# Kernel optimization log

Measured on AMD Instinct MI355X. Metric: run time of the kernel, lower is better.

## Reference

```python
import jax, jax.numpy as jnp
import numpy as np

NQ = 16  # nqubits
BATCH = 256

def _ry(t):
    # t: (...,) real angles -> (..., 2, 2) complex64 Ry(t)
    c = jnp.cos(t / 2).astype(jnp.complex64)
    s = jnp.sin(t / 2).astype(jnp.complex64)
    return jnp.stack([jnp.stack([c, -s], -1), jnp.stack([s, c], -1)], -2)

def _rz(t):
    # diag(e^{-i t/2}, e^{i t/2})
    e0 = jnp.exp(-0.5j * t.astype(jnp.complex64))
    e1 = jnp.exp(0.5j * t.astype(jnp.complex64))
    z = jnp.zeros_like(e0)
    return jnp.stack([jnp.stack([e0, z], -1), jnp.stack([z, e1], -1)], -2)

def _apply_1q(st, g, w):
    # st: (B, 2^n) complex, g: (2,2) or (B,2,2); wire w (0 = most significant, matching kron order)
    B = st.shape[0]
    x = st.reshape(B, 2 ** w, 2, -1)
    if g.ndim == 3:
        x = jnp.einsum('iab,ilbr->ilar', g, x)
    else:
        x = jnp.einsum('ab,ilbr->ilar', g, x)
    return x.reshape(B, -1)

def _apply_cnot(st, c, t, n):
    # CNOT(control=c, target=t): flip target bit where control bit == 1
    B = st.shape[0]
    x = st.reshape((B,) + (2,) * n)
    c_ax = c + 1
    ctrl0 = jnp.take(x, 0, axis=c_ax)
    ctrl1 = jnp.take(x, 1, axis=c_ax)
    t_ax = t + 1 if t < c else t  # target axis index after removing control axis
    ctrl1 = jnp.flip(ctrl1, axis=t_ax)  # flip along size-2 axis == Pauli-X
    x = jnp.stack([ctrl0, ctrl1], axis=c_ax)
    return x.reshape(B, -1)

def _yzy(st, w3, n):
    # per-qubit Ry(a) Rz(b) Ry(c); params laid out (n, 3) applied in order a, b, c
    p = w3.reshape(n, 3)
    g = jnp.einsum('nab,nbc,ncd->nad', _ry(p[:, 2]), _rz(p[:, 1]), _ry(p[:, 0]))
    for i in range(n):
        st = _apply_1q(st, g[i], i)
    return st

def _ring(st, step, n):
    # ring_of_cnot (step=1) / ring_of_cnot2 (step=2)
    for i in range(n):
        st = _apply_cnot(st, i, (i + step) % n, n)
    return st

def _forward(inputs, weight):
    B, n = inputs.shape
    # |0...0> initial state, batched
    st = jnp.zeros((B, 2 ** n), jnp.complex64).at[:, 0].set(1.0)
    # PauliEncoding with pauli='Y': Ry(inputs[:, i]) on wire i (batched gate)
    enc = _ry(inputs)  # (B, n, 2, 2)
    for i in range(n):
        st = _apply_1q(st, enc[:, i], i)
    # BasicEntangleLayer x2 = YZY + ring_of_cnot
    st = _yzy(st, weight[0 * n:3 * n], n); st = _ring(st, 1, n)
    st = _yzy(st, weight[3 * n:6 * n], n); st = _ring(st, 1, n)
    # YZY, ring_of_cnot2, YZY, ring_of_cnot2, YZY
    st = _yzy(st, weight[6 * n:9 * n], n); st = _ring(st, 2, n)
    st = _yzy(st, weight[9 * n:12 * n], n); st = _ring(st, 2, n)
    st = _yzy(st, weight[12 * n:15 * n], n)
    # <Z_i> = sum_probs(bit_i=0) - sum_probs(bit_i=1); output scaled by 4 as in original
    probs = st.real ** 2 + st.imag ** 2  # (B, 2^n) real
    z = []
    for i in range(n):
        p = probs.reshape(B, 2 ** i, 2, -1)
        z.append((p[:, :, 0, :] - p[:, :, 1, :]).sum(axis=(1, 2)))
    return jnp.stack(z, axis=1) * 4.0  # (B, n)

def setup_inputs() -> dict:
    key = jax.random.key(0)
    k1, k2 = jax.random.split(key)
    inputs = jax.random.uniform(k1, (BATCH, NQ), jnp.float32, 0.0, 2.0 * np.pi)
    weight = jax.random.uniform(k2, (15 * NQ,), jnp.float32, 0.0, 2.0 * np.pi)
    return {"inputs": inputs, "weight": weight}

def reference(inputs, weight):
    return _forward(inputs, weight)
```

## Files before the change

kernel.cpp:

```cpp
#include <hip/hip_runtime.h>
#include <hip/hip_fp16.h>
#include <utility>
#include <type_traits>


constexpr int NSR  = 88;
constexpr int NGRR = 22;
constexpr int NGL  = 10;
constexpr int NG   = 32;

struct M16 { unsigned r[16]; };

constexpr M16 ident() { M16 m{}; for (int i = 0; i < 16; ++i) m.r[i] = 1u << i; return m; }

constexpr M16 ringm(int s) {
  M16 m = ident();
  for (int i = 15; i >= 0; --i) {
    int pc = 15 - i;
    int pt = 15 - ((i + s) & 15);
    m.r[pt] ^= m.r[pc];
  }
  return m;
}

constexpr M16 mmul(M16 A, M16 B) {
  M16 C{};
  for (int p = 0; p < 16; ++p) {
    unsigned v = 0;
    for (int q = 0; q < 16; ++q) if ((A.r[p] >> q) & 1u) v ^= B.r[q];
    C.r[p] = v;
  }
  return C;
}

constexpr M16 minv(M16 A) {
  M16 I = ident();
  for (int col = 0; col < 16; ++col) {
    int piv = -1;
    for (int row = col; row < 16; ++row) if ((A.r[row] >> col) & 1u) { piv = row; break; }
    unsigned t = A.r[piv]; A.r[piv] = A.r[col]; A.r[col] = t;
    t = I.r[piv]; I.r[piv] = I.r[col]; I.r[col] = t;
    for (int row = 0; row < 16; ++row)
      if (row != col && ((A.r[row] >> col) & 1u)) { A.r[row] ^= A.r[col]; I.r[row] ^= I.r[col]; }
  }
  return I;
}

constexpr bool meq(M16 a, M16 b) { for (int i = 0; i < 16; ++i) if (a.r[i] != b.r[i]) return false; return true; }
constexpr unsigned colmask(M16 P, int b) { unsigned m = 0; for (int p = 0; p < 16; ++p) m |= ((P.r[p] >> b) & 1u) << p; return m; }
constexpr int popc16(unsigned x) { int c = 0; for (int i = 0; i < 16; ++i) c += (x >> i) & 1; return c; }
constexpr int topbit_pow(unsigned x) { int b = 0; for (int i = 0; i < 16; ++i) if ((x >> i) & 1) b = i; return 1 << b; }

struct Tables { unsigned gm[64]; unsigned gc[64]; unsigned meas[16]; };

constexpr Tables make_tables() {
  Tables T{};
  M16 R1 = ringm(1), R2 = ringm(2);
  M16 P0 = R1;
  M16 P1 = mmul(R1, R1);
  M16 P2 = mmul(P1, R2);
  M16 P3 = mmul(P2, R2);
  M16 P[4] = { P0, P1, P2, P3 };
  for (int k = 0; k < 4; ++k) {
    M16 A = minv(P[k]);
    for (int b = 0; b < 16; ++b) {
      T.gm[k * 16 + b] = colmask(P[k], b);
      T.gc[k * 16 + b] = A.r[b];
    }
  }
  M16 A5 = minv(P[3]);
  for (int w = 0; w < 16; ++w) T.meas[w] = A5.r[15 - w];
  return T;
}

constexpr Tables TB = make_tables();

constexpr bool check_tables() {
  for (int g = 0; g < 64; ++g) if ((popc16(TB.gm[g] & TB.gc[g]) & 1) != 1) return false;
  if (!meq(mmul(ringm(1), minv(ringm(1))), ident())) return false;
  if (!meq(mmul(ringm(2), minv(ringm(2))), ident())) return false;
  return true;
}
static_assert(check_tables(), "GF(2) table inconsistency");
static_assert(sizeof(__half2) == 4, "half2 size");

template<int N, int I = 0, typename F>
__device__ __forceinline__ void sfor(F&& f) {
  if constexpr (I < N) {
    f(std::integral_constant<int, I>{});
    sfor<N, I + 1>(static_cast<F&&>(f));
  }
}

__device__ __forceinline__ int h2i(__half2 v) { return __builtin_bit_cast(int, v); }
__device__ __forceinline__ __half2 i2h(int v) { return __builtin_bit_cast(__half2, v); }
__device__ __forceinline__ unsigned h2u(__half2 v) { return __builtin_bit_cast(unsigned, v); }
__device__ __forceinline__ __half2 u2h(unsigned v) { return __builtin_bit_cast(__half2, v); }

template<int T>
__device__ __forceinline__ __half2 upd(__half2 xs_, __half2 xp_,
                                       __half2 c0_, __half2 c1_, __half2 c2_, __half2 c3_) {
  const unsigned xs = h2u(xs_), xp = h2u(xp_);
  const unsigned c0 = h2u(c0_), c1 = h2u(c1_), c2 = h2u(c2_), c3 = h2u(c3_);
  unsigned y;
  if constexpr (T) {
    asm("v_pk_mul_f16 %0, %1, %2\n\t"
        "v_pk_fma_f16 %0, %3, %2, %0 op_sel:[0,1,0] op_sel_hi:[1,0,1] neg_lo:[1,0,0] neg_hi:[1,0,0]\n\t"
        "v_pk_fma_f16 %0, %4, %5, %0 neg_lo:[1,0,0] neg_hi:[1,0,0]\n\t"
        "v_pk_fma_f16 %0, %6, %5, %0 op_sel:[0,1,0] op_sel_hi:[1,0,1]"
        : "=&v"(y)
        : "v"(c0), "v"(xs), "v"(c1), "v"(c2), "v"(xp), "v"(c3));
  } else {
    asm("v_pk_mul_f16 %0, %1, %2\n\t"
        "v_pk_fma_f16 %0, %3, %2, %0 op_sel:[0,1,0] op_sel_hi:[1,0,1]\n\t"
        "v_pk_fma_f16 %0, %4, %5, %0\n\t"
        "v_pk_fma_f16 %0, %6, %5, %0 op_sel:[0,1,0] op_sel_hi:[1,0,1]"
        : "=&v"(y)
        : "v"(c0), "v"(xs), "v"(c1), "v"(c2), "v"(xp), "v"(c3));
  }
  return u2h(y);
}

template<int lx>
__device__ __forceinline__ __half2 pget(__half2 v) {
  if constexpr (lx == 0) return v;
  else return i2h(__shfl_xor(h2i(v), lx, 64));
}

__device__ __forceinline__ void su2_coeffs(float a, float b, float c,
                                           float& are, float& aim, float& bre, float& bim) {
  float sapc, capc, samc, camc, sb, cb;
  __sincosf((a + c) * 0.5f, &sapc, &capc);
  __sincosf((a - c) * 0.5f, &samc, &camc);
  __sincosf(b * 0.5f, &sb, &cb);
  are = cb * capc;
  aim = -sb * camc;
  bre = cb * sapc;
  bim = sb * samc;
}

__device__ __forceinline__ unsigned pkh2(float lo, float hi) {
  return h2u(__floats2half2_rn(lo, hi));
}

__device__ __forceinline__ float2 cmulf(float2 a, float vr, float vi) {
  return make_float2(a.x * vr - a.y * vi, a.x * vi + a.y * vr);
}

template<int G>
__device__ __forceinline__ void vg_load(const __half2 (&S)[NSR], const uint4* sg4,
                                        unsigned tid, __half2 (&a)[4]) {
  if constexpr (G < NGRR) {
    a[0] = S[4*G]; a[1] = S[4*G+1]; a[2] = S[4*G+2]; a[3] = S[4*G+3];
  } else {
    const uint4 v = sg4[(G - NGRR) * 512 + tid];
    a[0] = u2h(v.x); a[1] = u2h(v.y); a[2] = u2h(v.z); a[3] = u2h(v.w);
  }
}
template<int G>
__device__ __forceinline__ void vg_store(__half2 (&S)[NSR], uint4* sg4,
                                         unsigned tid, const __half2 (&a)[4]) {
  if constexpr (G < NGRR) {
    S[4*G] = a[0]; S[4*G+1] = a[1]; S[4*G+2] = a[2]; S[4*G+3] = a[3];
  } else {
    sg4[(G - NGRR) * 512 + tid] = make_uint4(h2u(a[0]), h2u(a[1]), h2u(a[2]), h2u(a[3]));
  }
}
template<int G>
__device__ __forceinline__ uint4 vg_pack(const __half2 (&S)[NSR], const uint4* sg4, unsigned tid) {
  if constexpr (G < NGRR)
    return make_uint4(h2u(S[4*G]), h2u(S[4*G+1]), h2u(S[4*G+2]), h2u(S[4*G+3]));
  else
    return sg4[(G - NGRR) * 512 + tid];
}

template<int G, int me, unsigned cm>
__device__ __forceinline__ void vg_upd(__half2 (&S)[NSR], uint4* sg4, unsigned tid, uint4 pv,
                                       __half2 c0, __half2 c1, __half2 c2, __half2 c3) {
  const unsigned q[4] = { pv.x, pv.y, pv.z, pv.w };
  __half2 a[4]; vg_load<G>(S, sg4, tid, a);
  sfor<4>([&](auto ee) {
    constexpr int e = decltype(ee)::value;
    constexpr int L = 4 * G + e;
    constexpr int t = popc16(cm & (unsigned)L) & 1;
    a[e] = upd<t>(a[e], u2h(q[e ^ me]), c0, c1, c2, c3);
  });
  vg_store<G>(S, sg4, tid, a);
}

template<int G>
__device__ __forceinline__ void apply_gate(__half2 (&S)[NSR], unsigned tid,
                                           const uint4* __restrict__ ctabg,
                                           uint4* sg4, uint4* xbuf4) {
  constexpr unsigned m  = TB.gm[G];
  constexpr unsigned c  = TB.gc[G];
  constexpr unsigned mL = m & 127u;
  constexpr unsigned mT = m >> 7;
  constexpr unsigned mW = m >> 13;

  const uint4 cc = ctabg[G];
  const unsigned fm = (__popc((c >> 7) & tid) & 1u) ? 0x80008000u : 0u;
  const __half2 c0 = u2h(cc.x), c1 = u2h(cc.y ^ fm), c2 = u2h(cc.z ^ fm), c3 = u2h(cc.w);

  if constexpr (mW == 0u) {
    constexpr int lx = (int)mT;
    if constexpr (mL == 0u) {
      sfor<NG>([&](auto gg) {
        constexpr int g = decltype(gg)::value;
        __half2 a[4]; vg_load<g>(S, sg4, tid, a);
        sfor<4>([&](auto ee) {
          constexpr int e = decltype(ee)::value;
          constexpr int L = 4*g + e;
          constexpr int t = popc16(c & (unsigned)L) & 1;
          a[e] = upd<t>(a[e], pget<lx>(a[e]), c0, c1, c2, c3);
        });
        vg_store<g>(S, sg4, tid, a);
      });
    } else if constexpr ((mL >> 2) == 0u) {
      constexpr int tb = topbit_pow(mL);
      sfor<NG>([&](auto gg) {
        constexpr int g = decltype(gg)::value;
        __half2 a[4]; vg_load<g>(S, sg4, tid, a);
        sfor<4>([&](auto ee) {
          constexpr int e = decltype(ee)::value;
          if constexpr ((e & tb) == 0) {
            constexpr int e1 = e ^ (int)mL;
            constexpr int L0 = 4*g + e, L1 = 4*g + e1;
            constexpr int t0 = popc16(c & (unsigned)L0) & 1;
            constexpr int t1 = popc16(c & (unsigned)L1) & 1;
            const __half2 x0 = a[e], x1 = a[e1];
            a[e]  = upd<t0>(x0, pget<lx>(x1), c0, c1, c2, c3);
            a[e1] = upd<t1>(x1, pget<lx>(x0), c0, c1, c2, c3);
          }
        });
        vg_store<g>(S, sg4, tid, a);
      });
    } else {
      constexpr int hg = (int)(mL >> 2);
      constexpr int tb = topbit_pow((unsigned)hg);
      constexpr int me = (int)(mL & 3u);
      sfor<NG>([&](auto ga_) {
        constexpr int gA = decltype(ga_)::value;
        if constexpr ((gA & tb) == 0) {
          constexpr int gB = gA ^ hg;
          __half2 a[4], b4[4];
          vg_load<gA>(S, sg4, tid, a); vg_load<gB>(S, sg4, tid, b4);
          sfor<4>([&](auto ee) {
            constexpr int e  = decltype(ee)::value;
            constexpr int e2 = e ^ me;
            constexpr int L0 = 4*gA + e, L1 = 4*gB + e2;
            constexpr int t0 = popc16(c & (unsigned)L0) & 1;
            constexpr int t1 = popc16(c & (unsigned)L1) & 1;
            const __half2 x0 = a[e], x1 = b4[e2];
            a[e]   = upd<t0>(x0, pget<lx>(x1), c0, c1, c2, c3);
            b4[e2] = upd<t1>(x1, pget<lx>(x0), c0, c1, c2, c3);
          });
          vg_store<gA>(S, sg4, tid, a); vg_store<gB>(S, sg4, tid, b4);
        }
      });
    }
  } else {
    const unsigned ptid = tid ^ (unsigned)mT;
    constexpr unsigned hG = mL >> 2;
    constexpr int      me = (int)(mL & 3u);
    if constexpr (hG == 0u) {
      sfor<4>([&](auto rr) {
        constexpr int r = decltype(rr)::value;
        sfor<8>([&](auto kk) {
          constexpr int k = decltype(kk)::value;
          xbuf4[tid * 9u + (unsigned)k] = vg_pack<r * 8 + k>(S, sg4, tid);
        });
        __syncthreads();
        sfor<8>([&](auto kk) {
          constexpr int k = decltype(kk)::value;
          const uint4 pv = xbuf4[ptid * 9u + (unsigned)k];
          vg_upd<r * 8 + k, me, c>(S, sg4, tid, pv, c0, c1, c2, c3);
        });
        __syncthreads();
      });
    } else {
      constexpr int tbG = topbit_pow(hG);
      sfor<4>([&](auto rr) {
        constexpr int r = decltype(rr)::value;
        sfor<4>([&](auto kk) {
          constexpr int k  = decltype(kk)::value;
          constexpr int i  = r * 4 + k;
          constexpr int gA = ((i & ~(tbG - 1)) << 1) | (i & (tbG - 1));
          constexpr int gB = gA ^ (int)hG;
          xbuf4[tid * 9u + (unsigned)k]       = vg_pack<gA>(S, sg4, tid);
          xbuf4[tid * 9u + (unsigned)(4 + k)] = vg_pack<gB>(S, sg4, tid);
        });
        __syncthreads();
        sfor<4>([&](auto kk) {
          constexpr int k  = decltype(kk)::value;
          constexpr int i  = r * 4 + k;
          constexpr int gA = ((i & ~(tbG - 1)) << 1) | (i & (tbG - 1));
          constexpr int gB = gA ^ (int)hG;
          const uint4 pvB = xbuf4[ptid * 9u + (unsigned)(4 + k)];
          const uint4 pvA = xbuf4[ptid * 9u + (unsigned)k];
          vg_upd<gA, me, c>(S, sg4, tid, pvB, c0, c1, c2, c3);
          vg_upd<gB, me, c>(S, sg4, tid, pvA, c0, c1, c2, c3);
        });
        __syncthreads();
      });
    }
  }
}

__global__ void ctab_build(const float* __restrict__ weight, uint4* __restrict__ ctabg) {
  const int g = (int)threadIdx.x;
  const int k = g >> 4;
  const int bb = g & 15;
  const int w = 15 - bb;
  const int base = 48 * (k + 1) + 3 * w;
  float are, aim, bre, bim;
  su2_coeffs(weight[base], weight[base + 1], weight[base + 2], are, aim, bre, bim);
  ctabg[g] = make_uint4(pkh2(are, are), pkh2(-aim, aim),
                        pkh2(-bre, -bre), pkh2(-bim, bim));
}

__global__ __attribute__((amdgpu_flat_work_group_size(512, 512)))
void qcir_kernel(const float* __restrict__ inputs, const float* __restrict__ weight,
                 float* __restrict__ out, const uint4* __restrict__ ctabg) {
  __shared__ uint4  sg4[NGL * 512];
  __shared__ uint4  xbuf4[512 * 9];
  __shared__ float4 itab[16];
  __shared__ float  red[8 * 16];

  const unsigned tid = threadIdx.x;
  const unsigned b   = blockIdx.x;

  if (tid < 16) {
    const int w = (int)tid;
    const float a = weight[3 * w] + inputs[b * 16 + w];
    float are, aim, bre, bim;
    su2_coeffs(a, weight[3 * w + 1], weight[3 * w + 2], are, aim, bre, bim);
    itab[w] = make_float4(are, aim, bre, bim);
  }
  __syncthreads();

  __half2 S[NSR];
  float2 P = make_float2(1.f, 0.f);
#pragma unroll
  for (int p = 7; p <= 15; ++p) {
    const int bit = (int)(tid >> (p - 7)) & 1;
    const float4 t = itab[15 - p];
    P = cmulf(P, bit ? t.z : t.x, bit ? t.w : t.y);
  }
  sfor<16>([&](auto hh) {
    constexpr int h = decltype(hh)::value;
    float2 ph = P;
    sfor<4>([&](auto qq) {
      constexpr int q   = decltype(qq)::value;
      constexpr int bit = (h >> q) & 1;
      const float4 t = itab[12 - q];
      if constexpr (bit) ph = cmulf(ph, t.z, t.w); else ph = cmulf(ph, t.x, t.y);
    });
    if constexpr (h < 11) {
      sfor<8>([&](auto ll) {
        constexpr int l = decltype(ll)::value;
        float2 pl = ph;
        sfor<3>([&](auto qq) {
          constexpr int q   = decltype(qq)::value;
          constexpr int bit = (l >> q) & 1;
          const float4 t = itab[15 - q];
          if constexpr (bit) pl = cmulf(pl, t.z, t.w); else pl = cmulf(pl, t.x, t.y);
        });
        S[h * 8 + l] = __floats2half2_rn(pl.x, pl.y);
      });
    } else {
      __half2 a0[4], a1[4];
      sfor<8>([&](auto ll) {
        constexpr int l = decltype(ll)::value;
        float2 pl = ph;
        sfor<3>([&](auto qq) {
          constexpr int q   = decltype(qq)::value;
          constexpr int bit = (l >> q) & 1;
          const float4 t = itab[15 - q];
          if constexpr (bit) pl = cmulf(pl, t.z, t.w); else pl = cmulf(pl, t.x, t.y);
        });
        const __half2 v = __floats2half2_rn(pl.x, pl.y);
        if constexpr (l < 4) a0[l] = v; else a1[l - 4] = v;
      });
      sg4[(2 * (h - 11)) * 512 + tid]     = make_uint4(h2u(a0[0]), h2u(a0[1]), h2u(a0[2]), h2u(a0[3]));
      sg4[(2 * (h - 11) + 1) * 512 + tid] = make_uint4(h2u(a1[0]), h2u(a1[1]), h2u(a1[2]), h2u(a1[3]));
    }
  });
  __syncthreads();

  sfor<64>([&](auto gg) { apply_gate<decltype(gg)::value>(S, tid, ctabg, sg4, xbuf4); });

  sfor<2>([&](auto hf_) {
    constexpr int hf = decltype(hf_)::value;
    float acc[8];
    sfor<8>([&](auto ww) { acc[decltype(ww)::value] = 0.f; });
    sfor<NSR>([&](auto ll) {
      constexpr int L = decltype(ll)::value;
      const float re = __low2float(S[L]);
      const float im = __high2float(S[L]);
      const float p = re * re + im * im;
      sfor<8>([&](auto w8) {
        constexpr int w = hf * 8 + decltype(w8)::value;
        constexpr int t = popc16(TB.meas[w] & 127u & (unsigned)L) & 1;
        if constexpr (t) acc[decltype(w8)::value] -= p; else acc[decltype(w8)::value] += p;
      });
    });
    sfor<NGL>([&](auto gg) {
      constexpr int g = decltype(gg)::value;
      const uint4 v = sg4[g * 512 + tid];
      const unsigned q[4] = { v.x, v.y, v.z, v.w };
      sfor<4>([&](auto ee) {
        constexpr int e = decltype(ee)::value;
        constexpr int L = NSR + g * 4 + e;
        const __half2 av = u2h(q[e]);
        const float re = __low2float(av);
        const float im = __high2float(av);
        const float p = re * re + im * im;
        sfor<8>([&](auto w8) {
          constexpr int w = hf * 8 + decltype(w8)::value;
          constexpr int t = popc16(TB.meas[w] & 127u & (unsigned)L) & 1;
          if constexpr (t) acc[decltype(w8)::value] -= p; else acc[decltype(w8)::value] += p;
        });
      });
    });
    sfor<8>([&](auto w8) {
      constexpr int w = hf * 8 + decltype(w8)::value;
      const unsigned fw = __popc((TB.meas[w] >> 7) & tid) & 1u;
      float z = fw ? -acc[decltype(w8)::value] : acc[decltype(w8)::value];
#pragma unroll
      for (int d = 1; d < 64; d <<= 1) z += __shfl_xor(z, d, 64);
      if ((tid & 63u) == 0u) red[(tid >> 6) * 16 + w] = z;
    });
  });
  __syncthreads();
  if (tid < 16) {
    float s = 0.f;
#pragma unroll
    for (int v = 0; v < 8; ++v) s += red[v * 16 + tid];
    out[b * 16 + tid] = 4.f * s;
  }
}

extern "C" void kernel_launch(void* const* d_in, const int* in_sizes, int n_in,
                              void* d_out, int out_size, void* d_ws, size_t ws_size,
                              hipStream_t stream) {
  const float* inputs = (const float*)d_in[0];
  const float* weight = (const float*)d_in[1];
  float* out = (float*)d_out;
  const int B = in_sizes[0] / 16;
  uint4* ctabg = reinterpret_cast<uint4*>(d_ws);
  ctab_build<<<1, 64, 0, stream>>>(weight, ctabg);
  qcir_kernel<<<B, 512, 0, stream>>>(inputs, weight, out, ctabg);
}
```

Measured before the change: 293.0 us.

## Keep more state in registers and interleave paired half2 gate updates

The number of half2 state groups kept in registers rises from 22 to 24 and the LDS-resident groups drop from 10 to 8, so fewer groups make shared-memory round trips in each gate. The single-amplitude update asm becomes a paired update that interleaves two independent packed-FMA chains, giving more instruction-level parallelism. To keep one asm block per pair, sign flips move from compile-time neg modifiers to precomputed positive and negated coefficient registers. Higher register pressure risks spills or lower occupancy.

```diff
diff --git a/kernel.cpp b/kernel.cpp
--- a/kernel.cpp
+++ b/kernel.cpp
@@ -4,9 +4,9 @@
 #include <type_traits>
 
 
-constexpr int NSR  = 88;
-constexpr int NGRR = 22;
-constexpr int NGL  = 10;
+constexpr int NSR  = 96;
+constexpr int NGRR = 24;
+constexpr int NGL  = 8;
 constexpr int NG   = 32;
 
 struct M16 { unsigned r[16]; };
@@ -97,28 +97,26 @@
 __device__ __forceinline__ unsigned h2u(__half2 v) { return __builtin_bit_cast(unsigned, v); }
 __device__ __forceinline__ __half2 u2h(unsigned v) { return __builtin_bit_cast(__half2, v); }
 
-template<int T>
-__device__ __forceinline__ __half2 upd(__half2 xs_, __half2 xp_,
-                                       __half2 c0_, __half2 c1_, __half2 c2_, __half2 c3_) {
-  const unsigned xs = h2u(xs_), xp = h2u(xp_);
-  const unsigned c0 = h2u(c0_), c1 = h2u(c1_), c2 = h2u(c2_), c3 = h2u(c3_);
-  unsigned y;
-  if constexpr (T) {
-    asm("v_pk_mul_f16 %0, %1, %2\n\t"
-        "v_pk_fma_f16 %0, %3, %2, %0 op_sel:[0,1,0] op_sel_hi:[1,0,1] neg_lo:[1,0,0] neg_hi:[1,0,0]\n\t"
-        "v_pk_fma_f16 %0, %4, %5, %0 neg_lo:[1,0,0] neg_hi:[1,0,0]\n\t"
-        "v_pk_fma_f16 %0, %6, %5, %0 op_sel:[0,1,0] op_sel_hi:[1,0,1]"
-        : "=&v"(y)
-        : "v"(c0), "v"(xs), "v"(c1), "v"(c2), "v"(xp), "v"(c3));
-  } else {
-    asm("v_pk_mul_f16 %0, %1, %2\n\t"
-        "v_pk_fma_f16 %0, %3, %2, %0 op_sel:[0,1,0] op_sel_hi:[1,0,1]\n\t"
-        "v_pk_fma_f16 %0, %4, %5, %0\n\t"
-        "v_pk_fma_f16 %0, %6, %5, %0 op_sel:[0,1,0] op_sel_hi:[1,0,1]"
-        : "=&v"(y)
-        : "v"(c0), "v"(xs), "v"(c1), "v"(c2), "v"(xp), "v"(c3));
-  }
-  return u2h(y);
+__device__ __forceinline__ void upd2(__half2& x0r, __half2& x1r,
+                                     __half2 xp0_, __half2 xp1_,
+                                     __half2 c0_, __half2 c1a_, __half2 c1b_,
+                                     __half2 c2a_, __half2 c2b_, __half2 c3_) {
+  const unsigned x0 = h2u(x0r), x1 = h2u(x1r), xp0 = h2u(xp0_), xp1 = h2u(xp1_);
+  const unsigned c0 = h2u(c0_), c1a = h2u(c1a_), c1b = h2u(c1b_),
+                 c2a = h2u(c2a_), c2b = h2u(c2b_), c3 = h2u(c3_);
+  unsigned y0, y1;
+  asm("v_pk_mul_f16 %0, %2, %3\n\t"
+      "v_pk_mul_f16 %1, %2, %4\n\t"
+      "v_pk_fma_f16 %0, %5, %3, %0 op_sel:[0,1,0] op_sel_hi:[1,0,1]\n\t"
+      "v_pk_fma_f16 %1, %6, %4, %1 op_sel:[0,1,0] op_sel_hi:[1,0,1]\n\t"
+      "v_pk_fma_f16 %0, %7, %9, %0\n\t"
+      "v_pk_fma_f16 %1, %8, %10, %1\n\t"
+      "v_pk_fma_f16 %0, %11, %9, %0 op_sel:[0,1,0] op_sel_hi:[1,0,1]\n\t"
+      "v_pk_fma_f16 %1, %11, %10, %1 op_sel:[0,1,0] op_sel_hi:[1,0,1]"
+      : "=&v"(y0), "=&v"(y1)
+      : "v"(c0), "v"(x0), "v"(x1), "v"(c1a), "v"(c1b),
+        "v"(c2a), "v"(c2b), "v"(xp0), "v"(xp1), "v"(c3));
+  x0r = u2h(y0); x1r = u2h(y1);
 }
 
 template<int lx>
@@ -176,15 +174,18 @@
 
 template<int G, int me, unsigned cm>
 __device__ __forceinline__ void vg_upd(__half2 (&S)[NSR], uint4* sg4, unsigned tid, uint4 pv,
-                                       __half2 c0, __half2 c1, __half2 c2, __half2 c3) {
+                                       __half2 c0, __half2 c1p, __half2 c1n,
+                                       __half2 c2p, __half2 c2n, __half2 c3) {
   const unsigned q[4] = { pv.x, pv.y, pv.z, pv.w };
   __half2 a[4]; vg_load<G>(S, sg4, tid, a);
-  sfor<4>([&](auto ee) {
-    constexpr int e = decltype(ee)::value;
-    constexpr int L = 4 * G + e;
-    constexpr int t = popc16(cm & (unsigned)L) & 1;
-    a[e] = upd<t>(a[e], u2h(q[e ^ me]), c0, c1, c2, c3);
-  });
+  constexpr int t0 = popc16(cm & (unsigned)(4*G+0)) & 1;
+  constexpr int t1 = popc16(cm & (unsigned)(4*G+1)) & 1;
+  constexpr int t2 = popc16(cm & (unsigned)(4*G+2)) & 1;
+  constexpr int t3 = popc16(cm & (unsigned)(4*G+3)) & 1;
+  upd2(a[0], a[1], u2h(q[0^me]), u2h(q[1^me]),
+       c0, t0?c1n:c1p, t1?c1n:c1p, t0?c2n:c2p, t1?c2n:c2p, c3);
+  upd2(a[2], a[3], u2h(q[2^me]), u2h(q[3^me]),
+       c0, t2?c1n:c1p, t3?c1n:c1p, t2?c2n:c2p, t3?c2n:c2p, c3);
   vg_store<G>(S, sg4, tid, a);
 }
 
@@ -200,7 +201,10 @@
 
   const uint4 cc = ctabg[G];
   const unsigned fm = (__popc((c >> 7) & tid) & 1u) ? 0x80008000u : 0u;
-  const __half2 c0 = u2h(cc.x), c1 = u2h(cc.y ^ fm), c2 = u2h(cc.z ^ fm), c3 = u2h(cc.w);
+  const unsigned c1u = cc.y ^ fm, c2u = cc.z ^ fm;
+  const __half2 c0 = u2h(cc.x), c3 = u2h(cc.w);
+  const __half2 c1p = u2h(c1u), c1n = u2h(c1u ^ 0x80008000u);
+  const __half2 c2p = u2h(c2u), c2n = u2h(c2u ^ 0x80008000u);
 
   if constexpr (mW == 0u) {
     constexpr int lx = (int)mT;
@@ -208,12 +212,14 @@
       sfor<NG>([&](auto gg) {
         constexpr int g = decltype(gg)::value;
         __half2 a[4]; vg_load<g>(S, sg4, tid, a);
-        sfor<4>([&](auto ee) {
-          constexpr int e = decltype(ee)::value;
-          constexpr int L = 4*g + e;
-          constexpr int t = popc16(c & (unsigned)L) & 1;
-          a[e] = upd<t>(a[e], pget<lx>(a[e]), c0, c1, c2, c3);
-        });
+        const __half2 p0 = pget<lx>(a[0]), p1 = pget<lx>(a[1]);
+        const __half2 p2 = pget<lx>(a[2]), p3 = pget<lx>(a[3]);
+        constexpr int t0 = popc16(c & (unsigned)(4*g+0)) & 1;
+        constexpr int t1 = popc16(c & (unsigned)(4*g+1)) & 1;
+        constexpr int t2 = popc16(c & (unsigned)(4*g+2)) & 1;
+        constexpr int t3 = popc16(c & (unsigned)(4*g+3)) & 1;
+        upd2(a[0], a[1], p0, p1, c0, t0?c1n:c1p, t1?c1n:c1p, t0?c2n:c2p, t1?c2n:c2p, c3);
+        upd2(a[2], a[3], p2, p3, c0, t2?c1n:c1p, t3?c1n:c1p, t2?c2n:c2p, t3?c2n:c2p, c3);
         vg_store<g>(S, sg4, tid, a);
       });
     } else if constexpr ((mL >> 2) == 0u) {
@@ -225,12 +231,11 @@
           constexpr int e = decltype(ee)::value;
           if constexpr ((e & tb) == 0) {
             constexpr int e1 = e ^ (int)mL;
-            constexpr int L0 = 4*g + e, L1 = 4*g + e1;
-            constexpr int t0 = popc16(c & (unsigned)L0) & 1;
-            constexpr int t1 = popc16(c & (unsigned)L1) & 1;
+            constexpr int t0 = popc16(c & (unsigned)(4*g+e)) & 1;
+            constexpr int t1 = popc16(c & (unsigned)(4*g+e1)) & 1;
             const __half2 x0 = a[e], x1 = a[e1];
-            a[e]  = upd<t0>(x0, pget<lx>(x1), c0, c1, c2, c3);
-            a[e1] = upd<t1>(x1, pget<lx>(x0), c0, c1, c2, c3);
+            upd2(a[e], a[e1], pget<lx>(x1), pget<lx>(x0),
+                 c0, t0?c1n:c1p, t1?c1n:c1p, t0?c2n:c2p, t1?c2n:c2p, c3);
           }
         });
         vg_store<g>(S, sg4, tid, a);
@@ -248,12 +253,11 @@
           sfor<4>([&](auto ee) {
             constexpr int e  = decltype(ee)::value;
             constexpr int e2 = e ^ me;
-            constexpr int L0 = 4*gA + e, L1 = 4*gB + e2;
-            constexpr int t0 = popc16(c & (unsigned)L0) & 1;
-            constexpr int t1 = popc16(c & (unsigned)L1) & 1;
+            constexpr int t0 = popc16(c & (unsigned)(4*gA+e)) & 1;
+            constexpr int t1 = popc16(c & (unsigned)(4*gB+e2)) & 1;
             const __half2 x0 = a[e], x1 = b4[e2];
-            a[e]   = upd<t0>(x0, pget<lx>(x1), c0, c1, c2, c3);
-            b4[e2] = upd<t1>(x1, pget<lx>(x0), c0, c1, c2, c3);
+            upd2(a[e], b4[e2], pget<lx>(x1), pget<lx>(x0),
+                 c0, t0?c1n:c1p, t1?c1n:c1p, t0?c2n:c2p, t1?c2n:c2p, c3);
           });
           vg_store<gA>(S, sg4, tid, a); vg_store<gB>(S, sg4, tid, b4);
         }
@@ -274,7 +278,7 @@
         sfor<8>([&](auto kk) {
           constexpr int k = decltype(kk)::value;
           const uint4 pv = xbuf4[ptid * 9u + (unsigned)k];
-          vg_upd<r * 8 + k, me, c>(S, sg4, tid, pv, c0, c1, c2, c3);
+          vg_upd<r * 8 + k, me, c>(S, sg4, tid, pv, c0, c1p, c1n, c2p, c2n, c3);
         });
         __syncthreads();
       });
@@ -298,8 +302,8 @@
           constexpr int gB = gA ^ (int)hG;
           const uint4 pvB = xbuf4[ptid * 9u + (unsigned)(4 + k)];
           const uint4 pvA = xbuf4[ptid * 9u + (unsigned)k];
-          vg_upd<gA, me, c>(S, sg4, tid, pvB, c0, c1, c2, c3);
-          vg_upd<gB, me, c>(S, sg4, tid, pvA, c0, c1, c2, c3);
+          vg_upd<gA, me, c>(S, sg4, tid, pvB, c0, c1p, c1n, c2p, c2n, c3);
+          vg_upd<gB, me, c>(S, sg4, tid, pvA, c0, c1p, c1n, c2p, c2n, c3);
         });
         __syncthreads();
       });
@@ -356,7 +360,7 @@
       const float4 t = itab[12 - q];
       if constexpr (bit) ph = cmulf(ph, t.z, t.w); else ph = cmulf(ph, t.x, t.y);
     });
-    if constexpr (h < 11) {
+    if constexpr (h < 12) {
       sfor<8>([&](auto ll) {
         constexpr int l = decltype(ll)::value;
         float2 pl = ph;
@@ -382,8 +386,8 @@
         const __half2 v = __floats2half2_rn(pl.x, pl.y);
         if constexpr (l < 4) a0[l] = v; else a1[l - 4] = v;
       });
-      sg4[(2 * (h - 11)) * 512 + tid]     = make_uint4(h2u(a0[0]), h2u(a0[1]), h2u(a0[2]), h2u(a0[3]));
-      sg4[(2 * (h - 11) + 1) * 512 + tid] = make_uint4(h2u(a1[0]), h2u(a1[1]), h2u(a1[2]), h2u(a1[3]));
+      sg4[(2 * (h - 12)) * 512 + tid]     = make_uint4(h2u(a0[0]), h2u(a0[1]), h2u(a0[2]), h2u(a0[3]));
+      sg4[(2 * (h - 12) + 1) * 512 + tid] = make_uint4(h2u(a1[0]), h2u(a1[1]), h2u(a1[2]), h2u(a1[3]));
     }
   });
   __syncthreads();
```

Result: faster. 279.0 us (-4.8%).
